# Kernel tuning notes

Hardware: AMD Instinct MI355X
Metric: run time of the kernel (lower is better)

Reference implementation:

```python
import jax, jax.numpy as jnp
import numpy as np

B, H, L, D = 4, 8, 2048, 64
FACTOR = 5
U = FACTOR * int(np.ceil(np.log(L)))  # sample_k == n_top == 40


def setup_inputs() -> dict:
    key = jax.random.key(0)
    kq, kk, kv, ki = jax.random.split(key, 4)
    return {
        "queries": jax.random.normal(kq, (B, L, H, D), dtype=jnp.float32),
        "keys": jax.random.normal(kk, (B, L, H, D), dtype=jnp.float32),
        "values": jax.random.normal(kv, (B, L, H, D), dtype=jnp.float32),
        "attn_mask": jnp.zeros((1,), dtype=bool),
        "random_index": jax.random.randint(ki, (L, U), 0, L),
    }


def _prob_attention(queries, keys, values, random_index):
    Bq, L_Q, Hq, Dq = queries.shape
    L_K = keys.shape[1]
    q = jnp.transpose(queries, (0, 2, 1, 3))  # [B,H,L_Q,D]
    k = jnp.transpose(keys, (0, 2, 1, 3))     # [B,H,L_K,D]
    v = jnp.transpose(values, (0, 2, 1, 3))   # [B,H,L_V,D]
    n_top = min(FACTOR * int(np.ceil(np.log(L_Q))), L_Q)

    # --- ProbSparse query scoring: sample K per query, M = max - mean ---
    k_samp = k[:, :, random_index, :]                        # [B,H,L_Q,S,D] gather
    qk_samp = jnp.einsum('bhqd,bhqsd->bhqs', q, k_samp)      # [B,H,L_Q,S]
    M = qk_samp.max(axis=-1) - qk_samp.sum(axis=-1) / L_K    # [B,H,L_Q]
    _, top_idx = jax.lax.top_k(M, n_top)                     # [B,H,n_top]

    # --- dense scores only for the top queries ---
    q_sel = jnp.take_along_axis(q, top_idx[..., None], axis=2)  # [B,H,n_top,D]
    scale = 1.0 / jnp.sqrt(jnp.asarray(Dq, jnp.float32))        # self.scale or 1/sqrt(D)
    scores = jnp.einsum('bhud,bhkd->bhuk', q_sel, k) * scale    # [B,H,n_top,L_K]

    # --- ProbMask: causal mask rows gathered at selected query positions ---
    causal = jnp.triu(jnp.ones((L_Q, L_K), dtype=bool), 1)
    scores = jnp.where(causal[top_idx], -jnp.inf, scores)
    attn = jax.nn.softmax(scores, axis=-1)

    # --- initial context = cumsum(V) (mask_flag=True), scatter updates ---
    ctx = jnp.cumsum(v, axis=2)                              # [B,H,L_Q,D]
    upd = jnp.einsum('bhuk,bhkd->bhud', attn, v)             # [B,H,n_top,D]
    b_idx = jnp.arange(Bq)[:, None, None]
    h_idx = jnp.arange(Hq)[None, :, None]
    ctx = ctx.at[b_idx, h_idx, top_idx].set(upd)
    return jnp.transpose(ctx, (0, 2, 1, 3))                  # [B,L_Q,H,D]


def reference(queries, keys, values, attn_mask, random_index):
    # attn_mask is ignored by the torch module (it builds its own ProbMask).
    return _prob_attention(queries, keys, values, random_index)
```

## Files before the change

kernel.cpp:

```cpp
#include <hip/hip_runtime.h>

#define Bd 4
#define Hd 8
#define Ld 2048
#define Dd 64
#define Ud 40
#define NTOP 40
#define NCHUNK 128
#define CSZ 16

#define NS 16
#define FTILE 128
#define QSTR 68
#define KSTR 68
#define PSTR 132

__global__ __launch_bounds__(256) void compute_M_kernel(
    const float* __restrict__ q, const float* __restrict__ k,
    const int* __restrict__ ridx, float* __restrict__ M) {
  const int nblk = Bd * Ld / 4;
  int orig = blockIdx.x;
  int bid = (orig & 7) * (nblk >> 3) + (orig >> 3);
  int gw = bid * 4 + (threadIdx.x >> 6);
  int lane = threadIdx.x & 63;
  int hg = lane >> 3;
  int s8 = lane & 7;
  int b = gw >> 11;
  int l = gw & (Ld - 1);

  const float* qrow = q + ((size_t)b * Ld + l) * (Hd * Dd) + lane * 8;
  float4 q0 = *reinterpret_cast<const float4*>(qrow);
  float4 q1 = *reinterpret_cast<const float4*>(qrow + 4);

  int rv = 0;
  if (lane < Ud) rv = ridx[l * Ud + lane];

  const float* kb = k + (size_t)b * Ld * (Hd * Dd);

  float mx = -INFINITY, sm = 0.f;
#pragma unroll 8
  for (int u = 0; u < Ud; ++u) {
    int kidx = __shfl(rv, u);
    const float* kr = kb + (size_t)kidx * (Hd * Dd) + lane * 8;
    float4 k0 = *reinterpret_cast<const float4*>(kr);
    float4 k1 = *reinterpret_cast<const float4*>(kr + 4);
    float dot = q0.x * k0.x + q0.y * k0.y + q0.z * k0.z + q0.w * k0.w +
                q1.x * k1.x + q1.y * k1.y + q1.z * k1.z + q1.w * k1.w;
    dot += __shfl_xor(dot, 1);
    dot += __shfl_xor(dot, 2);
    dot += __shfl_xor(dot, 4);
    mx = fmaxf(mx, dot);
    sm += dot;
  }
  if (s8 == 0)
    M[((size_t)b * Hd + hg) * Ld + l] = mx - sm * (1.0f / (float)Ld);
}

__global__ __launch_bounds__(64) void topk_kernel(const float* __restrict__ M,
                                                  int* __restrict__ topIdx) {
  int bh = blockIdx.x;
  int lane = threadIdx.x;
  const float* mrow = M + (size_t)bh * Ld;

  unsigned int key[32];
#pragma unroll
  for (int j = 0; j < 32; ++j) {
    unsigned int bits = __float_as_uint(mrow[lane + j * 64]);
    key[j] = (bits & 0x80000000u) ? ~bits : (bits | 0x80000000u);
  }

  const int ISENT = 1 << 30;
  unsigned int k0 = 0u, k1c = 0u, k2c = 0u;
  int i0 = ISENT, i1c = ISENT, i2c = ISENT;
#pragma unroll
  for (int j = 0; j < 32; ++j) {
    unsigned int kj = key[j];
    int idx = lane + j * 64;
    if (kj > k0) {
      k2c = k1c; i2c = i1c; k1c = k0; i1c = i0; k0 = kj; i0 = idx;
    } else if (kj > k1c) {
      k2c = k1c; i2c = i1c; k1c = kj; i1c = idx;
    } else if (kj > k2c) {
      k2c = kj; i2c = idx;
    }
  }

  for (int it = 0; it < NTOP; ++it) {
    unsigned int wk = k0;
    int wi = i0;
#pragma unroll
    for (int off = 1; off < 64; off <<= 1) {
      unsigned int ok = __shfl_xor(wk, off);
      int oi = __shfl_xor(wi, off);
      if (ok > wk || (ok == wk && oi < wi)) { wk = ok; wi = oi; }
    }
    if (lane == 0) topIdx[bh * NTOP + it] = wi;
    if (wi == i0) {
      k0 = k1c; i0 = i1c; k1c = k2c; i1c = i2c; k2c = 0u; i2c = ISENT;
      if (k0 == 0u) {
        i0 = ISENT; i1c = ISENT; i2c = ISENT;
#pragma unroll
        for (int j = 0; j < 32; ++j) {
          unsigned int kj = key[j];
          int idx = lane + j * 64;
          bool valid = (kj < wk) || (kj == wk && idx > wi);
          kj = valid ? kj : 0u;
          if (kj > k0) {
            k2c = k1c; i2c = i1c; k1c = k0; i1c = i0; k0 = kj; i0 = idx;
          } else if (kj > k1c) {
            k2c = k1c; i2c = i1c; k1c = kj; i1c = idx;
          } else if (kj > k2c) {
            k2c = kj; i2c = idx;
          }
        }
      }
    }
  }
}

__global__ void chunk_sums_kernel(const float* __restrict__ v,
                                  float* __restrict__ csum) {
  __shared__ float red[256];
  int blk = blockIdx.x;
  int c = blk % NCHUNK, bh = blk / NCHUNK;
  int b = bh >> 3, h = bh & 7;
  int d = threadIdx.x & 63, jg = threadIdx.x >> 6;
  int t0 = c * CSZ;
  float s = 0.f;
#pragma unroll
  for (int j = jg; j < CSZ; j += 4)
    s += v[(((size_t)b * Ld + t0 + j) * Hd + h) * Dd + d];
  red[threadIdx.x] = s;
  __syncthreads();
  if (jg == 0)
    csum[(size_t)blk * Dd + d] = red[d] + red[64 + d] + red[128 + d] + red[192 + d];
}

__global__ void scan_chunks_kernel(float* __restrict__ csum) {
  int bh = blockIdx.x;
  int d = threadIdx.x;
  float acc = 0.f;
#pragma unroll 8
  for (int c = 0; c < NCHUNK; ++c) {
    size_t i = ((size_t)bh * NCHUNK + c) * Dd + d;
    float s = csum[i];
    csum[i] = acc;
    acc += s;
  }
}

__global__ void cumsum_write_kernel(const float* __restrict__ v,
                                    const float* __restrict__ csum,
                                    float* __restrict__ out) {
  int blk = blockIdx.x;
  int c = blk % NCHUNK, bh = blk / NCHUNK;
  int b = bh >> 3, h = bh & 7;
  int d = threadIdx.x;
  float acc = csum[(size_t)blk * Dd + d];
  int t0 = c * CSZ;
#pragma unroll 4
  for (int j = 0; j < CSZ; ++j) {
    size_t idx = (((size_t)b * Ld + t0 + j) * Hd + h) * Dd + d;
    acc += v[idx];
    out[idx] = acc;
  }
}

__global__ __launch_bounds__(256) void flash_attn_kernel(
    const float* __restrict__ q, const float* __restrict__ k,
    const float* __restrict__ v, const int* __restrict__ topIdx,
    float* __restrict__ Opart, float* __restrict__ mS,
    float* __restrict__ sS) {
  __shared__ float qs[NTOP * QSTR];
  __shared__ float ks[FTILE * KSTR];
  __shared__ float p[NTOP * PSTR];
  __shared__ int ts[NTOP];
  int tid = threadIdx.x;
  int split = blockIdx.x % NS;
  int bh = blockIdx.x / NS;
  int b = bh >> 3, h = bh & 7;
  int k0 = split * FTILE;

  if (tid < NTOP) ts[tid] = topIdx[bh * NTOP + tid];
  __syncthreads();

  for (int i = tid; i < NTOP * 16; i += 256) {
    int u = i >> 4, ps = i & 15;
    float4 qv = reinterpret_cast<const float4*>(
        q + (((size_t)b * Ld + ts[u]) * Hd + h) * Dd)[ps];
    *reinterpret_cast<float4*>(&qs[u * QSTR + ps * 4]) = qv;
  }
  for (int i = tid; i < FTILE * 16; i += 256) {
    int r = i >> 4, ps = i & 15;
    float4 kv = reinterpret_cast<const float4*>(
        k + (((size_t)b * Ld + k0 + r) * Hd + h) * Dd)[ps];
    *reinterpret_cast<float4*>(&ks[r * KSTR + ps * 4]) = kv;
  }
  __syncthreads();

  int ug = tid & 7, kg = tid >> 3;
  int ub = ug * 5, kb = kg * 4;
  {
    float acc[5][4] = {};
    for (int dd = 0; dd < Dd; dd += 4) {
      float4 kv[4], qv[5];
#pragma unroll
      for (int i = 0; i < 4; ++i)
        kv[i] = *reinterpret_cast<const float4*>(&ks[(kb + i) * KSTR + dd]);
#pragma unroll
      for (int i = 0; i < 5; ++i)
        qv[i] = *reinterpret_cast<const float4*>(&qs[(ub + i) * QSTR + dd]);
#pragma unroll
      for (int ui = 0; ui < 5; ++ui)
#pragma unroll
        for (int ki = 0; ki < 4; ++ki)
          acc[ui][ki] += qv[ui].x * kv[ki].x + qv[ui].y * kv[ki].y +
                         qv[ui].z * kv[ki].z + qv[ui].w * kv[ki].w;
    }
#pragma unroll
    for (int ui = 0; ui < 5; ++ui) {
      int u = ub + ui;
      int t = ts[u];
      float4 o;
      o.x = (k0 + kb + 0 <= t) ? acc[ui][0] * 0.125f : -INFINITY;
      o.y = (k0 + kb + 1 <= t) ? acc[ui][1] * 0.125f : -INFINITY;
      o.z = (k0 + kb + 2 <= t) ? acc[ui][2] * 0.125f : -INFINITY;
      o.w = (k0 + kb + 3 <= t) ? acc[ui][3] * 0.125f : -INFINITY;
      *reinterpret_cast<float4*>(&p[u * PSTR + kb]) = o;
    }
  }
  __syncthreads();

  for (int i = tid; i < FTILE * 16; i += 256) {
    int r = i >> 4, ps = i & 15;
    float4 vv = reinterpret_cast<const float4*>(
        v + (((size_t)b * Ld + k0 + r) * Hd + h) * Dd)[ps];
    *reinterpret_cast<float4*>(&ks[r * KSTR + ps * 4]) = vv;
  }
  if (tid < NTOP * 4) {
    int u = tid >> 2, l4 = tid & 3;
    float* pr = p + u * PSTR;
    float mx = -1e30f;
#pragma unroll 8
    for (int j = l4; j < FTILE; j += 4) mx = fmaxf(mx, pr[j]);
    mx = fmaxf(mx, __shfl_xor(mx, 1));
    mx = fmaxf(mx, __shfl_xor(mx, 2));
    float sum = 0.f;
#pragma unroll 8
    for (int j = l4; j < FTILE; j += 4) {
      float pe = __expf(pr[j] - mx);
      pr[j] = pe;
      sum += pe;
    }
    sum += __shfl_xor(sum, 1);
    sum += __shfl_xor(sum, 2);
    if (l4 == 0) {
      mS[((size_t)bh * NS + split) * NTOP + u] = mx;
      sS[((size_t)bh * NS + split) * NTOP + u] = sum;
    }
  }
  __syncthreads();

  int ug2 = tid >> 5, dg = tid & 31;
  int ub2 = ug2 * 5, d2 = dg * 2;
  float acc[5][2] = {};
#pragma unroll 4
  for (int kk = 0; kk < FTILE; ++kk) {
    float2 vv = *reinterpret_cast<const float2*>(&ks[kk * KSTR + d2]);
#pragma unroll
    for (int i = 0; i < 5; ++i) {
      float pe = p[(ub2 + i) * PSTR + kk];
      acc[i][0] += pe * vv.x;
      acc[i][1] += pe * vv.y;
    }
  }
  float* ob = Opart + ((size_t)bh * NS + split) * (NTOP * Dd);
#pragma unroll
  for (int i = 0; i < 5; ++i)
    *reinterpret_cast<float2*>(&ob[(ub2 + i) * Dd + d2]) =
        make_float2(acc[i][0], acc[i][1]);
}

__global__ __launch_bounds__(64) void flash_combine_kernel(
    const float* __restrict__ Opart, const float* __restrict__ mS,
    const float* __restrict__ sS, const int* __restrict__ topIdx,
    float* __restrict__ out) {
  int row = blockIdx.x;
  int u = row % NTOP, bh = row / NTOP;
  int b = bh >> 3, h = bh & 7;
  int d = threadIdx.x;
  int t = topIdx[row];

  float mg = -1e30f;
#pragma unroll
  for (int s = 0; s < NS; ++s)
    mg = fmaxf(mg, mS[((size_t)bh * NS + s) * NTOP + u]);
  float den = 0.f, o = 0.f;
#pragma unroll
  for (int s = 0; s < NS; ++s) {
    float w = __expf(mS[((size_t)bh * NS + s) * NTOP + u] - mg);
    den += w * sS[((size_t)bh * NS + s) * NTOP + u];
    o += w * Opart[(((size_t)bh * NS + s) * NTOP + u) * Dd + d];
  }
  out[(((size_t)b * Ld + t) * Hd + h) * Dd + d] = o / den;
}

__global__ void attn_update_kernel(const float* __restrict__ q,
                                   const float* __restrict__ k,
                                   const float* __restrict__ v,
                                   const int* __restrict__ topIdx,
                                   float* __restrict__ out) {
  __shared__ float sc[Ld];
  __shared__ float qs[Dd];
  __shared__ float red[256];
  int tid = threadIdx.x;
  int bh = blockIdx.x / NTOP;
  int b = bh >> 3, h = bh & 7;
  int t = topIdx[blockIdx.x];

  if (tid < Dd) qs[tid] = q[(((size_t)b * Ld + t) * Hd + h) * Dd + tid];
  __syncthreads();

  int nk = t + 1;
  const float4* qv4 = reinterpret_cast<const float4*>(qs);
  float lmax = -INFINITY;
  for (int kk = tid; kk < nk; kk += 256) {
    const float4* kr = reinterpret_cast<const float4*>(
        k + (((size_t)b * Ld + kk) * Hd + h) * Dd);
    float dot = 0.f;
#pragma unroll
    for (int j = 0; j < Dd / 4; ++j) {
      float4 a = qv4[j];
      float4 bb = kr[j];
      dot += a.x * bb.x + a.y * bb.y + a.z * bb.z + a.w * bb.w;
    }
    dot *= 0.125f;
    sc[kk] = dot;
    lmax = fmaxf(lmax, dot);
  }
  red[tid] = lmax;
  __syncthreads();
  for (int s = 128; s; s >>= 1) {
    if (tid < s) red[tid] = fmaxf(red[tid], red[tid + s]);
    __syncthreads();
  }
  float m = red[0];
  __syncthreads();
  float lsum = 0.f;
  for (int kk = tid; kk < nk; kk += 256) {
    float pp = __expf(sc[kk] - m);
    sc[kk] = pp;
    lsum += pp;
  }
  red[tid] = lsum;
  __syncthreads();
  for (int s = 128; s; s >>= 1) {
    if (tid < s) red[tid] += red[tid + s];
    __syncthreads();
  }
  float inv_denom = 1.0f / red[0];
  __syncthreads();
  int d = tid & 63, kg = tid >> 6;
  float acc = 0.f;
  for (int kk = kg; kk < nk; kk += 4)
    acc += sc[kk] * v[(((size_t)b * Ld + kk) * Hd + h) * Dd + d];
  red[tid] = acc;
  __syncthreads();
  if (kg == 0) {
    float r = red[d] + red[64 + d] + red[128 + d] + red[192 + d];
    out[(((size_t)b * Ld + t) * Hd + h) * Dd + d] = r * inv_denom;
  }
}

extern "C" void kernel_launch(void* const* d_in, const int* in_sizes, int n_in,
                              void* d_out, int out_size, void* d_ws,
                              size_t ws_size, hipStream_t stream) {
  const float* q = (const float*)d_in[0];
  const float* k = (const float*)d_in[1];
  const float* v = (const float*)d_in[2];
  const int* ridx = (const int*)d_in[4];
  float* out = (float*)d_out;

  char* ws = (char*)d_ws;
  float* M = (float*)(ws + 0);
  int* topIdx = (int*)(ws + 262144);
  float* csum = (float*)(ws + 272384);
  float* Opart = (float*)(ws + 3942400);
  float* mS = (float*)(ws + 9185280);
  float* sS = (float*)(ws + 9267200);
  const size_t need_new = 9349120;

  compute_M_kernel<<<Bd * Ld / 4, 256, 0, stream>>>(q, k, ridx, M);
  topk_kernel<<<Bd * Hd, 64, 0, stream>>>(M, topIdx);
  chunk_sums_kernel<<<Bd * Hd * NCHUNK, 256, 0, stream>>>(v, csum);
  scan_chunks_kernel<<<Bd * Hd, 64, 0, stream>>>(csum);
  cumsum_write_kernel<<<Bd * Hd * NCHUNK, 64, 0, stream>>>(v, csum, out);

  if (ws_size >= need_new) {
    flash_attn_kernel<<<Bd * Hd * NS, 256, 0, stream>>>(q, k, v, topIdx,
                                                        Opart, mS, sS);
    flash_combine_kernel<<<Bd * Hd * NTOP, 64, 0, stream>>>(Opart, mS, sS,
                                                            topIdx, out);
  } else {
    attn_update_kernel<<<Bd * Hd * NTOP, 256, 0, stream>>>(q, k, v, topIdx, out);
  }
}
```

Measured before the change: 108.7 us.

## Merge independent stages into three heterogeneous launches to cut kernel count

Merges independent work into shared launches. M scoring and V chunk sums share phase1, top-k and the chunk scan share phase2, and the flash attention partials and cumsum write share phase3, with each block branching on its block index. This cuts the pipeline from seven launches to four and lets independent stages overlap on the GPU. Chunks grow from 16 to 32 rows, giving half as many chunk sums, and the cumsum write now packs four chunks per 256-thread block. The cost is extra branching and shared-memory allocation in the merged blocks, and the 2048-block and 512-block offsets are hardcoded.

Measured after the change: 94.77 us, median of 3. -12.8%, faster.

```diff
diff --git a/kernel.cpp b/kernel.cpp
--- a/kernel.cpp
+++ b/kernel.cpp
@@ -6,8 +6,8 @@
 #define Dd 64
 #define Ud 40
 #define NTOP 40
-#define NCHUNK 128
-#define CSZ 16
+#define NCHUNK 64
+#define CSZ 32
 
 #define NS 16
 #define FTILE 128
@@ -15,160 +15,145 @@
 #define KSTR 68
 #define PSTR 132
 
-__global__ __launch_bounds__(256) void compute_M_kernel(
+__global__ __launch_bounds__(256) void phase1_kernel(
     const float* __restrict__ q, const float* __restrict__ k,
-    const int* __restrict__ ridx, float* __restrict__ M) {
-  const int nblk = Bd * Ld / 4;
-  int orig = blockIdx.x;
-  int bid = (orig & 7) * (nblk >> 3) + (orig >> 3);
-  int gw = bid * 4 + (threadIdx.x >> 6);
-  int lane = threadIdx.x & 63;
-  int hg = lane >> 3;
-  int s8 = lane & 7;
-  int b = gw >> 11;
-  int l = gw & (Ld - 1);
-
-  const float* qrow = q + ((size_t)b * Ld + l) * (Hd * Dd) + lane * 8;
-  float4 q0 = *reinterpret_cast<const float4*>(qrow);
-  float4 q1 = *reinterpret_cast<const float4*>(qrow + 4);
-
-  int rv = 0;
-  if (lane < Ud) rv = ridx[l * Ud + lane];
-
-  const float* kb = k + (size_t)b * Ld * (Hd * Dd);
-
-  float mx = -INFINITY, sm = 0.f;
-#pragma unroll 8
-  for (int u = 0; u < Ud; ++u) {
-    int kidx = __shfl(rv, u);
-    const float* kr = kb + (size_t)kidx * (Hd * Dd) + lane * 8;
-    float4 k0 = *reinterpret_cast<const float4*>(kr);
-    float4 k1 = *reinterpret_cast<const float4*>(kr + 4);
-    float dot = q0.x * k0.x + q0.y * k0.y + q0.z * k0.z + q0.w * k0.w +
-                q1.x * k1.x + q1.y * k1.y + q1.z * k1.z + q1.w * k1.w;
-    dot += __shfl_xor(dot, 1);
-    dot += __shfl_xor(dot, 2);
-    dot += __shfl_xor(dot, 4);
-    mx = fmaxf(mx, dot);
-    sm += dot;
-  }
-  if (s8 == 0)
-    M[((size_t)b * Hd + hg) * Ld + l] = mx - sm * (1.0f / (float)Ld);
-}
-
-__global__ __launch_bounds__(64) void topk_kernel(const float* __restrict__ M,
-                                                  int* __restrict__ topIdx) {
-  int bh = blockIdx.x;
+    const float* __restrict__ v, const int* __restrict__ ridx,
+    float* __restrict__ M, float* __restrict__ csum) {
+  __shared__ float red[256];
+  int tid = threadIdx.x;
+  if (blockIdx.x < 2048) {
+    const int nblk = 2048;
+    int orig = blockIdx.x;
+    int bid = (orig & 7) * (nblk >> 3) + (orig >> 3);
+    int gw = bid * 4 + (tid >> 6);
+    int lane = tid & 63;
+    int hg = lane >> 3;
+    int s8 = lane & 7;
+    int b = gw >> 11;
+    int l = gw & (Ld - 1);
+
+    const float* qrow = q + ((size_t)b * Ld + l) * (Hd * Dd) + lane * 8;
+    float4 q0 = *reinterpret_cast<const float4*>(qrow);
+    float4 q1 = *reinterpret_cast<const float4*>(qrow + 4);
+
+    int rv = 0;
+    if (lane < Ud) rv = ridx[l * Ud + lane];
+    const float* kb = k + (size_t)b * Ld * (Hd * Dd);
+
+    float mx = -INFINITY, sm = 0.f;
+#pragma unroll 8
+    for (int u = 0; u < Ud; ++u) {
+      int kidx = __shfl(rv, u);
+      const float* kr = kb + (size_t)kidx * (Hd * Dd) + lane * 8;
+      float4 k0 = *reinterpret_cast<const float4*>(kr);
+      float4 k1 = *reinterpret_cast<const float4*>(kr + 4);
+      float dot = q0.x * k0.x + q0.y * k0.y + q0.z * k0.z + q0.w * k0.w +
+                  q1.x * k1.x + q1.y * k1.y + q1.z * k1.z + q1.w * k1.w;
+      dot += __shfl_xor(dot, 1);
+      dot += __shfl_xor(dot, 2);
+      dot += __shfl_xor(dot, 4);
+      mx = fmaxf(mx, dot);
+      sm += dot;
+    }
+    if (s8 == 0)
+      M[((size_t)b * Hd + hg) * Ld + l] = mx - sm * (1.0f / (float)Ld);
+  } else {
+    int n = blockIdx.x - 2048;
+    int c = n & (NCHUNK - 1), bh = n >> 6;
+    int b = bh >> 3, h = bh & 7;
+    int d = tid & 63, jg = tid >> 6;
+    int t0 = c * CSZ;
+    float s = 0.f;
+#pragma unroll
+    for (int j = jg; j < CSZ; j += 4)
+      s += v[(((size_t)b * Ld + t0 + j) * Hd + h) * Dd + d];
+    red[tid] = s;
+    __syncthreads();
+    if (jg == 0)
+      csum[(size_t)n * Dd + d] =
+          red[d] + red[64 + d] + red[128 + d] + red[192 + d];
+  }
+}
+
+__global__ __launch_bounds__(64) void phase2_kernel(const float* __restrict__ M,
+                                                    int* __restrict__ topIdx,
+                                                    float* __restrict__ csum) {
   int lane = threadIdx.x;
-  const float* mrow = M + (size_t)bh * Ld;
-
-  unsigned int key[32];
-#pragma unroll
-  for (int j = 0; j < 32; ++j) {
-    unsigned int bits = __float_as_uint(mrow[lane + j * 64]);
-    key[j] = (bits & 0x80000000u) ? ~bits : (bits | 0x80000000u);
-  }
-
-  const int ISENT = 1 << 30;
-  unsigned int k0 = 0u, k1c = 0u, k2c = 0u;
-  int i0 = ISENT, i1c = ISENT, i2c = ISENT;
-#pragma unroll
-  for (int j = 0; j < 32; ++j) {
-    unsigned int kj = key[j];
-    int idx = lane + j * 64;
-    if (kj > k0) {
-      k2c = k1c; i2c = i1c; k1c = k0; i1c = i0; k0 = kj; i0 = idx;
-    } else if (kj > k1c) {
-      k2c = k1c; i2c = i1c; k1c = kj; i1c = idx;
-    } else if (kj > k2c) {
-      k2c = kj; i2c = idx;
-    }
-  }
-
-  for (int it = 0; it < NTOP; ++it) {
-    unsigned int wk = k0;
-    int wi = i0;
-#pragma unroll
-    for (int off = 1; off < 64; off <<= 1) {
-      unsigned int ok = __shfl_xor(wk, off);
-      int oi = __shfl_xor(wi, off);
-      if (ok > wk || (ok == wk && oi < wi)) { wk = ok; wi = oi; }
-    }
-    if (lane == 0) topIdx[bh * NTOP + it] = wi;
-    if (wi == i0) {
-      k0 = k1c; i0 = i1c; k1c = k2c; i1c = i2c; k2c = 0u; i2c = ISENT;
-      if (k0 == 0u) {
-        i0 = ISENT; i1c = ISENT; i2c = ISENT;
-#pragma unroll
-        for (int j = 0; j < 32; ++j) {
-          unsigned int kj = key[j];
-          int idx = lane + j * 64;
-          bool valid = (kj < wk) || (kj == wk && idx > wi);
-          kj = valid ? kj : 0u;
-          if (kj > k0) {
-            k2c = k1c; i2c = i1c; k1c = k0; i1c = i0; k0 = kj; i0 = idx;
-          } else if (kj > k1c) {
-            k2c = k1c; i2c = i1c; k1c = kj; i1c = idx;
-          } else if (kj > k2c) {
-            k2c = kj; i2c = idx;
+  if (blockIdx.x < 32) {
+    int bh = blockIdx.x;
+    const float* mrow = M + (size_t)bh * Ld;
+
+    unsigned int key[32];
+#pragma unroll
+    for (int j = 0; j < 32; ++j) {
+      unsigned int bits = __float_as_uint(mrow[lane + j * 64]);
+      key[j] = (bits & 0x80000000u) ? ~bits : (bits | 0x80000000u);
+    }
+
+    const int ISENT = 1 << 30;
+    unsigned int k0 = 0u, k1c = 0u, k2c = 0u;
+    int i0 = ISENT, i1c = ISENT, i2c = ISENT;
+#pragma unroll
+    for (int j = 0; j < 32; ++j) {
+      unsigned int kj = key[j];
+      int idx = lane + j * 64;
+      if (kj > k0) {
+        k2c = k1c; i2c = i1c; k1c = k0; i1c = i0; k0 = kj; i0 = idx;
+      } else if (kj > k1c) {
+        k2c = k1c; i2c = i1c; k1c = kj; i1c = idx;
+      } else if (kj > k2c) {
+        k2c = kj; i2c = idx;
+      }
+    }
+
+    for (int it = 0; it < NTOP; ++it) {
+      unsigned int wk = k0;
+      int wi = i0;
+#pragma unroll
+      for (int off = 1; off < 64; off <<= 1) {
+        unsigned int ok = __shfl_xor(wk, off);
+        int oi = __shfl_xor(wi, off);
+        if (ok > wk || (ok == wk && oi < wi)) { wk = ok; wi = oi; }
+      }
+      if (lane == 0) topIdx[bh * NTOP + it] = wi;
+      if (wi == i0) {
+        k0 = k1c; i0 = i1c; k1c = k2c; i1c = i2c; k2c = 0u; i2c = ISENT;
+        if (k0 == 0u) {
+          i0 = ISENT; i1c = ISENT; i2c = ISENT;
+#pragma unroll
+          for (int j = 0; j < 32; ++j) {
+            unsigned int kj = key[j];
+            int idx = lane + j * 64;
+            bool valid = (kj < wk) || (kj == wk && idx > wi);
+            kj = valid ? kj : 0u;
+            if (kj > k0) {
+              k2c = k1c; i2c = i1c; k1c = k0; i1c = i0; k0 = kj; i0 = idx;
+            } else if (kj > k1c) {
+              k2c = k1c; i2c = i1c; k1c = kj; i1c = idx;
+            } else if (kj > k2c) {
+              k2c = kj; i2c = idx;
+            }
           }
         }
       }
     }
-  }
-}
-
-__global__ void chunk_sums_kernel(const float* __restrict__ v,
-                                  float* __restrict__ csum) {
-  __shared__ float red[256];
-  int blk = blockIdx.x;
-  int c = blk % NCHUNK, bh = blk / NCHUNK;
-  int b = bh >> 3, h = bh & 7;
-  int d = threadIdx.x & 63, jg = threadIdx.x >> 6;
-  int t0 = c * CSZ;
-  float s = 0.f;
-#pragma unroll
-  for (int j = jg; j < CSZ; j += 4)
-    s += v[(((size_t)b * Ld + t0 + j) * Hd + h) * Dd + d];
-  red[threadIdx.x] = s;
-  __syncthreads();
-  if (jg == 0)
-    csum[(size_t)blk * Dd + d] = red[d] + red[64 + d] + red[128 + d] + red[192 + d];
-}
-
-__global__ void scan_chunks_kernel(float* __restrict__ csum) {
-  int bh = blockIdx.x;
-  int d = threadIdx.x;
-  float acc = 0.f;
-#pragma unroll 8
-  for (int c = 0; c < NCHUNK; ++c) {
-    size_t i = ((size_t)bh * NCHUNK + c) * Dd + d;
-    float s = csum[i];
-    csum[i] = acc;
-    acc += s;
-  }
-}
-
-__global__ void cumsum_write_kernel(const float* __restrict__ v,
-                                    const float* __restrict__ csum,
-                                    float* __restrict__ out) {
-  int blk = blockIdx.x;
-  int c = blk % NCHUNK, bh = blk / NCHUNK;
-  int b = bh >> 3, h = bh & 7;
-  int d = threadIdx.x;
-  float acc = csum[(size_t)blk * Dd + d];
-  int t0 = c * CSZ;
-#pragma unroll 4
-  for (int j = 0; j < CSZ; ++j) {
-    size_t idx = (((size_t)b * Ld + t0 + j) * Hd + h) * Dd + d;
-    acc += v[idx];
-    out[idx] = acc;
-  }
-}
-
-__global__ __launch_bounds__(256) void flash_attn_kernel(
+  } else {
+    int bh = blockIdx.x - 32;
+    float acc = 0.f;
+#pragma unroll 8
+    for (int c = 0; c < NCHUNK; ++c) {
+      size_t i = ((size_t)bh * NCHUNK + c) * Dd + lane;
+      float s = csum[i];
+      csum[i] = acc;
+      acc += s;
+    }
+  }
+}
+
+__global__ __launch_bounds__(256) void phase3_kernel(
     const float* __restrict__ q, const float* __restrict__ k,
     const float* __restrict__ v, const int* __restrict__ topIdx,
+    const float* __restrict__ csum, float* __restrict__ out,
     float* __restrict__ Opart, float* __restrict__ mS,
     float* __restrict__ sS) {
   __shared__ float qs[NTOP * QSTR];
@@ -176,6 +161,25 @@
   __shared__ float p[NTOP * PSTR];
   __shared__ int ts[NTOP];
   int tid = threadIdx.x;
+
+  if (blockIdx.x >= 512) {
+    int m = blockIdx.x - 512;
+    int lane = tid & 63, w = tid >> 6;
+    int blk = m * 4 + w;
+    int c = blk & (NCHUNK - 1), bh = blk >> 6;
+    int b = bh >> 3, h = bh & 7;
+    float acc = csum[(size_t)blk * Dd + lane];
+    int t0 = c * CSZ;
+    const float* vp = v + (((size_t)b * Ld + t0) * Hd + h) * Dd + lane;
+    float* op = out + (((size_t)b * Ld + t0) * Hd + h) * Dd + lane;
+#pragma unroll 8
+    for (int j = 0; j < CSZ; ++j) {
+      acc += vp[(size_t)j * (Hd * Dd)];
+      op[(size_t)j * (Hd * Dd)] = acc;
+    }
+    return;
+  }
+
   int split = blockIdx.x % NS;
   int bh = blockIdx.x / NS;
   int b = bh >> 3, h = bh & 7;
@@ -303,6 +307,23 @@
     o += w * Opart[(((size_t)bh * NS + s) * NTOP + u) * Dd + d];
   }
   out[(((size_t)b * Ld + t) * Hd + h) * Dd + d] = o / den;
+}
+
+__global__ void cumsum_write_kernel(const float* __restrict__ v,
+                                    const float* __restrict__ csum,
+                                    float* __restrict__ out) {
+  int blk = blockIdx.x;
+  int c = blk & (NCHUNK - 1), bh = blk >> 6;
+  int b = bh >> 3, h = bh & 7;
+  int d = threadIdx.x;
+  float acc = csum[(size_t)blk * Dd + d];
+  int t0 = c * CSZ;
+#pragma unroll 8
+  for (int j = 0; j < CSZ; ++j) {
+    size_t idx = (((size_t)b * Ld + t0 + j) * Hd + h) * Dd + d;
+    acc += v[idx];
+    out[idx] = acc;
+  }
 }
 
 __global__ void attn_update_kernel(const float* __restrict__ q,
@@ -390,18 +411,17 @@
   float* sS = (float*)(ws + 9267200);
   const size_t need_new = 9349120;
 
-  compute_M_kernel<<<Bd * Ld / 4, 256, 0, stream>>>(q, k, ridx, M);
-  topk_kernel<<<Bd * Hd, 64, 0, stream>>>(M, topIdx);
-  chunk_sums_kernel<<<Bd * Hd * NCHUNK, 256, 0, stream>>>(v, csum);
-  scan_chunks_kernel<<<Bd * Hd, 64, 0, stream>>>(csum);
-  cumsum_write_kernel<<<Bd * Hd * NCHUNK, 64, 0, stream>>>(v, csum, out);
+  phase1_kernel<<<4096, 256, 0, stream>>>(q, k, v, ridx, M, csum);
+  phase2_kernel<<<64, 64, 0, stream>>>(M, topIdx, csum);
 
   if (ws_size >= need_new) {
-    flash_attn_kernel<<<Bd * Hd * NS, 256, 0, stream>>>(q, k, v, topIdx,
-                                                        Opart, mS, sS);
+    phase3_kernel<<<1024, 256, 0, stream>>>(q, k, v, topIdx, csum, out, Opart,
+                                            mS, sS);
     flash_combine_kernel<<<Bd * Hd * NTOP, 64, 0, stream>>>(Opart, mS, sS,
                                                             topIdx, out);
   } else {
-    attn_update_kernel<<<Bd * Hd * NTOP, 256, 0, stream>>>(q, k, v, topIdx, out);
-  }
-}
+    cumsum_write_kernel<<<Bd * Hd * NCHUNK, 64, 0, stream>>>(v, csum, out);
+    attn_update_kernel<<<Bd * Hd * NTOP, 256, 0, stream>>>(q, k, v, topIdx,
+                                                           out);
+  }
+}
```
